# Optimization experiments

Hardware: AMD Instinct MI355X
Metric: run time of the kernel (lower is better)

## Reference

```python
import jax, jax.numpy as jnp
import numpy as np
from jax import lax

B, N, C, H, W = 8, 256, 512, 8, 8
DIM = C * 2  # 1024
HW = H * W


def setup_inputs() -> dict:
    key = jax.random.key(0)
    ks = jax.random.split(key, 8)
    x = jax.random.normal(ks[0], (B, N, C, H, W), dtype=jnp.float32)
    # 3 frozen conv1d(1,1,k=5) layers: kaiming-normal weights, zero bias
    conv_w = jax.random.normal(ks[1], (3, 5), dtype=jnp.float32) * np.float32(np.sqrt(2.0 / 5.0))
    conv_b = jnp.zeros((3,), dtype=jnp.float32)
    # 512 tiny Linear(HW, 2): weight [out,in] stacked -> [C, 2, HW], trunc-normal std=0.01
    Ws = (jax.random.truncated_normal(ks[2], -2.0, 2.0, (C, 2, HW), dtype=jnp.float32) * 0.01)
    bs = jnp.zeros((C, 2), dtype=jnp.float32)
    # frozen fc Linear(DIM, DIM)
    fc_w = (jax.random.truncated_normal(ks[3], -2.0, 2.0, (DIM, DIM), dtype=jnp.float32) * 0.01)
    fc_b = jnp.zeros((DIM,), dtype=jnp.float32)
    return {"x": x, "conv_w": conv_w, "conv_b": conv_b, "Ws": Ws, "bs": bs, "fc_w": fc_w, "fc_b": fc_b}


def _conv1d_same(a, w, b):
    # a: [B, N], w: [5], b: scalar; cross-correlation with padding 2 (same as torch Conv1d)
    out = lax.conv_general_dilated(a[:, None, :], w[None, None, :], (1,), [(2, 2)])
    return out[:, 0, :] + b


def reference(x, conv_w, conv_b, Ws, bs, fc_w, fc_b):
    # Channel (patch) attention loop, 3 iterations
    for i in range(3):
        att = x.mean(axis=(2, 3, 4))                      # AdaptiveAvgPool1d(1) over (C H W) -> [B, N]
        att = jax.nn.sigmoid(_conv1d_same(att, conv_w[i], conv_b[i]))  # [B, N]
        x = x * att[:, :, None, None, None]
    xf = x.reshape(B, N, C, HW)
    # 512 per-channel Linear(HW, 2) as one grouped contraction
    y = jnp.einsum('bnch,coh->bnco', xf, Ws) + bs          # [B, N, C, 2]
    y = y.reshape(B, N, C * 2)                             # [B, N, 1024]
    out = y @ fc_w.T + fc_b                                # frozen fc
    # dropout in eval mode = identity
    return out
```

## Files before the change

### kernel.cpp

```cpp
#include <hip/hip_runtime.h>
#include <hip/hip_bf16.h>


typedef unsigned short u16;
typedef __attribute__((ext_vector_type(8))) short short8;
typedef __attribute__((ext_vector_type(4))) float floatx4;

#define Bb 8
#define Nn 256
#define Cc 512
#define HWs 64
#define BN 2048
#define DIMd 1024

__device__ inline u16 f2bf(float f) {
    unsigned int u = __builtin_bit_cast(unsigned int, f);
    unsigned int r = (u + 0x7FFFu + ((u >> 16) & 1u)) >> 16;
    return (u16)r;
}

__global__ __launch_bounds__(256) void k1_reduce_grouped(
    const float* __restrict__ x, const float* __restrict__ Ws,
    float* __restrict__ yprime, float* __restrict__ m0)
{
    const int bid = blockIdx.x;
    const int tid = threadIdx.x;
    const float* xb = x + (size_t)bid * (Cc * HWs);
    const int q = tid & 3;
    const int cofs = tid >> 2;
    float lsum = 0.f;

    for (int p = 0; p < 8; ++p) {
        const int c = p * 64 + cofs;
        const floatx4* xp  = (const floatx4*)(xb + p * 4096 + tid * 16);
        const floatx4* w0p = (const floatx4*)(Ws + (size_t)(c * 2 + 0) * HWs + q * 16);
        const floatx4* w1p = (const floatx4*)(Ws + (size_t)(c * 2 + 1) * HWs + q * 16);
        float d0 = 0.f, d1 = 0.f;
        #pragma unroll
        for (int v = 0; v < 4; ++v) {
            floatx4 xv = xp[v];
            floatx4 w0 = w0p[v];
            floatx4 w1 = w1p[v];
            #pragma unroll
            for (int j = 0; j < 4; ++j) {
                d0 += xv[j] * w0[j];
                d1 += xv[j] * w1[j];
                lsum += xv[j];
            }
        }
        d0 += __shfl_xor(d0, 1); d0 += __shfl_xor(d0, 2);
        d1 += __shfl_xor(d1, 1); d1 += __shfl_xor(d1, 2);
        if (q == 0) {
            yprime[(size_t)bid * DIMd + c * 2 + 0] = d0;
            yprime[(size_t)bid * DIMd + c * 2 + 1] = d1;
        }
    }
    #pragma unroll
    for (int s = 32; s; s >>= 1) lsum += __shfl_xor(lsum, s);
    __shared__ float wsum[4];
    if ((tid & 63) == 0) wsum[tid >> 6] = lsum;
    __syncthreads();
    if (tid == 0)
        m0[bid] = (wsum[0] + wsum[1] + wsum[2] + wsum[3]) * (1.0f / 32768.f);
}

__global__ __launch_bounds__(256) void k2_scale(
    const float* __restrict__ m0, const float* __restrict__ conv_w,
    const float* __restrict__ conv_b, float* __restrict__ scale)
{
    const int b = blockIdx.x;
    const int n = threadIdx.x;
    __shared__ float buf[Nn];
    float a = m0[b * Nn + n];
    float p = 1.f;
    for (int i = 0; i < 3; ++i) {
        buf[n] = a;
        __syncthreads();
        float t = 0.f;
        #pragma unroll
        for (int k = 0; k < 5; ++k) {
            int idx = n + k - 2;
            float v = (idx >= 0 && idx < Nn) ? buf[idx] : 0.f;
            t += v * conv_w[i * 5 + k];
        }
        t += conv_b[i];
        float s = 1.f / (1.f + __expf(-t));
        p *= s;
        a *= s;
        __syncthreads();
    }
    scale[b * Nn + n] = p;
}

__global__ __launch_bounds__(256) void k3_gemm(
    const float* __restrict__ yprime, const float* __restrict__ scale,
    const float* __restrict__ bs, const float* __restrict__ fc_w,
    const float* __restrict__ fc_b, float* __restrict__ out)
{
    const int tid = threadIdx.x;
    const int w = tid >> 6;
    const int lane = tid & 63;
    const int l15 = lane & 15;
    const int quad = lane >> 4;
    const int wm = w & 1, wn = w >> 1;
    const int r0 = blockIdx.x * 64 + wm * 32;
    const int c0 = blockIdx.y * 64 + wn * 32;

    floatx4 acc[2][2] = {};
    const int rowA0 = r0 + l15;
    const float sc0 = scale[rowA0];
    const float sc1 = scale[rowA0 + 16];

    for (int k0 = 0; k0 < DIMd; k0 += 32) {
        const int ka = k0 + quad * 8;
        const floatx4* bsp = (const floatx4*)(bs + ka);
        floatx4 bs0 = bsp[0], bs1 = bsp[1];
        short8 afr[2], bfr[2];
        #pragma unroll
        for (int mi = 0; mi < 2; ++mi) {
            const int row = rowA0 + mi * 16;
            const floatx4* yp = (const floatx4*)(yprime + (size_t)row * DIMd + ka);
            floatx4 y0 = yp[0], y1 = yp[1];
            const float sc = mi ? sc1 : sc0;
            short8 af;
            #pragma unroll
            for (int j = 0; j < 4; ++j) af[j]     = (short)f2bf(sc * y0[j] + bs0[j]);
            #pragma unroll
            for (int j = 0; j < 4; ++j) af[4 + j] = (short)f2bf(sc * y1[j] + bs1[j]);
            afr[mi] = af;
        }
        #pragma unroll
        for (int ni = 0; ni < 2; ++ni) {
            const int col = c0 + ni * 16 + l15;
            const floatx4* bp = (const floatx4*)(fc_w + (size_t)col * DIMd + ka);
            floatx4 b0 = bp[0], b1 = bp[1];
            short8 bf;
            #pragma unroll
            for (int j = 0; j < 4; ++j) { bf[j] = (short)f2bf(b0[j]); bf[4 + j] = (short)f2bf(b1[j]); }
            bfr[ni] = bf;
        }
        #pragma unroll
        for (int mi = 0; mi < 2; ++mi)
            #pragma unroll
            for (int ni = 0; ni < 2; ++ni)
                acc[mi][ni] = __builtin_amdgcn_mfma_f32_16x16x32_bf16(afr[mi], bfr[ni], acc[mi][ni], 0, 0, 0);
    }

    #pragma unroll
    for (int ni = 0; ni < 2; ++ni) {
        const int col = c0 + ni * 16 + l15;
        const float fb = fc_b[col];
        #pragma unroll
        for (int mi = 0; mi < 2; ++mi) {
            #pragma unroll
            for (int r = 0; r < 4; ++r) {
                const int row = r0 + mi * 16 + quad * 4 + r;
                out[(size_t)row * DIMd + col] = acc[mi][ni][r] + fb;
            }
        }
    }
}

extern "C" void kernel_launch(void* const* d_in, const int* in_sizes, int n_in,
                              void* d_out, int out_size, void* d_ws, size_t ws_size,
                              hipStream_t stream) {
    const float* x      = (const float*)d_in[0];
    const float* conv_w = (const float*)d_in[1];
    const float* conv_b = (const float*)d_in[2];
    const float* Ws     = (const float*)d_in[3];
    const float* bs     = (const float*)d_in[4];
    const float* fc_w   = (const float*)d_in[5];
    const float* fc_b   = (const float*)d_in[6];
    float* out = (float*)d_out;

    float* m0     = (float*)d_ws;
    float* scale  = m0 + BN;
    float* yprime = scale + BN;

    k1_reduce_grouped<<<dim3(BN), dim3(256), 0, stream>>>(x, Ws, yprime, m0);
    k2_scale<<<dim3(Bb), dim3(Nn), 0, stream>>>(m0, conv_w, conv_b, scale);
    k3_gemm<<<dim3(32, 16), dim3(256), 0, stream>>>(yprime, scale, bs, fc_w, fc_b, out);
}
```

Baseline: 449.0 us.

## Move per-row scale and bias out of GEMM inner loop; prestore bf16 operands

After: 423.4 us. -5.7%, faster.

```diff
diff --git a/kernel.cpp b/kernel.cpp
--- a/kernel.cpp
+++ b/kernel.cpp
@@ -3,6 +3,7 @@
 
 
 typedef unsigned short u16;
+typedef unsigned int u32;
 typedef __attribute__((ext_vector_type(8))) short short8;
 typedef __attribute__((ext_vector_type(4))) float floatx4;
 
@@ -19,9 +20,40 @@
     return (u16)r;
 }
 
+__global__ __launch_bounds__(256) void k0a_cvt_w(
+    const float* __restrict__ w, u16* __restrict__ wb)
+{
+    const int i = blockIdx.x * 256 + threadIdx.x;
+    floatx4 v = ((const floatx4*)w)[i];
+    u32 lo = (u32)f2bf(v[0]) | ((u32)f2bf(v[1]) << 16);
+    u32 hi = (u32)f2bf(v[2]) | ((u32)f2bf(v[3]) << 16);
+    ((u32*)wb)[i * 2 + 0] = lo;
+    ((u32*)wb)[i * 2 + 1] = hi;
+}
+
+__global__ __launch_bounds__(256) void k0b_bias(
+    const float* __restrict__ bs, const float* __restrict__ fc_w,
+    const float* __restrict__ fc_b, float* __restrict__ bias2)
+{
+    const int wv = blockIdx.x * 4 + (threadIdx.x >> 6);
+    const int lane = threadIdx.x & 63;
+    const floatx4* bp = (const floatx4*)(fc_w + (size_t)wv * DIMd + lane * 16);
+    const floatx4* sp = (const floatx4*)(bs + lane * 16);
+    float s = 0.f;
+    #pragma unroll
+    for (int v = 0; v < 4; ++v) {
+        floatx4 a = bp[v], b = sp[v];
+        #pragma unroll
+        for (int j = 0; j < 4; ++j) s += a[j] * b[j];
+    }
+    #pragma unroll
+    for (int sft = 32; sft; sft >>= 1) s += __shfl_xor(s, sft);
+    if (lane == 0) bias2[wv] = s + fc_b[wv];
+}
+
 __global__ __launch_bounds__(256) void k1_reduce_grouped(
     const float* __restrict__ x, const float* __restrict__ Ws,
-    float* __restrict__ yprime, float* __restrict__ m0)
+    u16* __restrict__ ybf, float* __restrict__ m0)
 {
     const int bid = blockIdx.x;
     const int tid = threadIdx.x;
@@ -51,8 +83,8 @@
         d0 += __shfl_xor(d0, 1); d0 += __shfl_xor(d0, 2);
         d1 += __shfl_xor(d1, 1); d1 += __shfl_xor(d1, 2);
         if (q == 0) {
-            yprime[(size_t)bid * DIMd + c * 2 + 0] = d0;
-            yprime[(size_t)bid * DIMd + c * 2 + 1] = d1;
+            u32 pk = (u32)f2bf(d0) | ((u32)f2bf(d1) << 16);
+            ((u32*)ybf)[(size_t)bid * (DIMd / 2) + c] = pk;
         }
     }
     #pragma unroll
@@ -93,9 +125,9 @@
 }
 
 __global__ __launch_bounds__(256) void k3_gemm(
-    const float* __restrict__ yprime, const float* __restrict__ scale,
-    const float* __restrict__ bs, const float* __restrict__ fc_w,
-    const float* __restrict__ fc_b, float* __restrict__ out)
+    const u16* __restrict__ ybf, const u16* __restrict__ wbf,
+    const float* __restrict__ scale, const float* __restrict__ bias2,
+    float* __restrict__ out)
 {
     const int tid = threadIdx.x;
     const int w = tid >> 6;
@@ -107,55 +139,32 @@
     const int c0 = blockIdx.y * 64 + wn * 32;
 
     floatx4 acc[2][2] = {};
-    const int rowA0 = r0 + l15;
-    const float sc0 = scale[rowA0];
-    const float sc1 = scale[rowA0 + 16];
+    const u16* aptr0 = ybf + (size_t)(r0 + l15) * DIMd + quad * 8;
+    const u16* aptr1 = aptr0 + 16 * DIMd;
+    const u16* bptr0 = wbf + (size_t)(c0 + l15) * DIMd + quad * 8;
+    const u16* bptr1 = bptr0 + 16 * DIMd;
 
     for (int k0 = 0; k0 < DIMd; k0 += 32) {
-        const int ka = k0 + quad * 8;
-        const floatx4* bsp = (const floatx4*)(bs + ka);
-        floatx4 bs0 = bsp[0], bs1 = bsp[1];
-        short8 afr[2], bfr[2];
-        #pragma unroll
-        for (int mi = 0; mi < 2; ++mi) {
-            const int row = rowA0 + mi * 16;
-            const floatx4* yp = (const floatx4*)(yprime + (size_t)row * DIMd + ka);
-            floatx4 y0 = yp[0], y1 = yp[1];
-            const float sc = mi ? sc1 : sc0;
-            short8 af;
-            #pragma unroll
-            for (int j = 0; j < 4; ++j) af[j]     = (short)f2bf(sc * y0[j] + bs0[j]);
-            #pragma unroll
-            for (int j = 0; j < 4; ++j) af[4 + j] = (short)f2bf(sc * y1[j] + bs1[j]);
-            afr[mi] = af;
-        }
-        #pragma unroll
-        for (int ni = 0; ni < 2; ++ni) {
-            const int col = c0 + ni * 16 + l15;
-            const floatx4* bp = (const floatx4*)(fc_w + (size_t)col * DIMd + ka);
-            floatx4 b0 = bp[0], b1 = bp[1];
-            short8 bf;
-            #pragma unroll
-            for (int j = 0; j < 4; ++j) { bf[j] = (short)f2bf(b0[j]); bf[4 + j] = (short)f2bf(b1[j]); }
-            bfr[ni] = bf;
-        }
-        #pragma unroll
-        for (int mi = 0; mi < 2; ++mi)
-            #pragma unroll
-            for (int ni = 0; ni < 2; ++ni)
-                acc[mi][ni] = __builtin_amdgcn_mfma_f32_16x16x32_bf16(afr[mi], bfr[ni], acc[mi][ni], 0, 0, 0);
+        short8 a0 = *(const short8*)(aptr0 + k0);
+        short8 a1 = *(const short8*)(aptr1 + k0);
+        short8 b0 = *(const short8*)(bptr0 + k0);
+        short8 b1 = *(const short8*)(bptr1 + k0);
+        acc[0][0] = __builtin_amdgcn_mfma_f32_16x16x32_bf16(a0, b0, acc[0][0], 0, 0, 0);
+        acc[0][1] = __builtin_amdgcn_mfma_f32_16x16x32_bf16(a0, b1, acc[0][1], 0, 0, 0);
+        acc[1][0] = __builtin_amdgcn_mfma_f32_16x16x32_bf16(a1, b0, acc[1][0], 0, 0, 0);
+        acc[1][1] = __builtin_amdgcn_mfma_f32_16x16x32_bf16(a1, b1, acc[1][1], 0, 0, 0);
     }
 
     #pragma unroll
     for (int ni = 0; ni < 2; ++ni) {
         const int col = c0 + ni * 16 + l15;
-        const float fb = fc_b[col];
+        const float b2 = bias2[col];
         #pragma unroll
         for (int mi = 0; mi < 2; ++mi) {
             #pragma unroll
             for (int r = 0; r < 4; ++r) {
                 const int row = r0 + mi * 16 + quad * 4 + r;
-                out[(size_t)row * DIMd + col] = acc[mi][ni][r] + fb;
+                out[(size_t)row * DIMd + col] = scale[row] * acc[mi][ni][r] + b2;
             }
         }
     }
@@ -173,11 +182,15 @@
     const float* fc_b   = (const float*)d_in[6];
     float* out = (float*)d_out;
 
-    float* m0     = (float*)d_ws;
-    float* scale  = m0 + BN;
-    float* yprime = scale + BN;
+    float* m0    = (float*)d_ws;
+    float* scale = m0 + BN;
+    float* bias2 = scale + BN;
+    u16*   ybf   = (u16*)(bias2 + DIMd);
+    u16*   wbf   = ybf + (size_t)BN * DIMd;
 
-    k1_reduce_grouped<<<dim3(BN), dim3(256), 0, stream>>>(x, Ws, yprime, m0);
+    k0a_cvt_w<<<dim3(1024), dim3(256), 0, stream>>>(fc_w, wbf);
+    k0b_bias<<<dim3(256), dim3(256), 0, stream>>>(bs, fc_w, fc_b, bias2);
+    k1_reduce_grouped<<<dim3(BN), dim3(256), 0, stream>>>(x, Ws, ybf, m0);
     k2_scale<<<dim3(Bb), dim3(Nn), 0, stream>>>(m0, conv_w, conv_b, scale);
-    k3_gemm<<<dim3(32, 16), dim3(256), 0, stream>>>(yprime, scale, bs, fc_w, fc_b, out);
+    k3_gemm<<<dim3(32, 16), dim3(256), 0, stream>>>(ybf, wbf, scale, bias2, out);
 }
```
